# Optimization experiments

Measured on AMD Instinct MI355X. Metric: run time of the kernel, lower is better.

Reference implementation:

```python
import jax, jax.numpy as jnp
import numpy as np

N = 262144          # particles
E = N * 32          # neighbor pairs (edges)


def wendland(q, h):
    # 2D Wendland C2 kernel, q = r/h in [0,1]
    C = 7.0 / (np.pi) / (h * h)
    b = jnp.clip(1.0 - q, 0.0, None)
    return C * (b ** 4) * (1.0 + 4.0 * q)


def setup_inputs() -> dict:
    key = jax.random.key(0)
    k1, k2, k3, k4, k5 = jax.random.split(key, 5)
    area = jax.random.uniform(k1, (N,), jnp.float32) * 0.5 + 0.5
    density = jax.random.uniform(k2, (N,), jnp.float32) * 0.2 + 0.9
    restDensity = jnp.ones((N,), jnp.float32) * 998.0
    velocity = jax.random.normal(k3, (N, 2), jnp.float32)
    radialDistance = jax.random.uniform(k4, (E,), jnp.float32)
    neighbors = jax.random.randint(k5, (2, E), 0, N, jnp.int64)
    return {
        "fluidCoefficient": jnp.float32(0.01),
        "area": area,
        "density": density,
        "restDensity": restDensity,
        "velocity": velocity,
        "radialDistance": radialDistance,
        "neighbors": neighbors,
        "support": jnp.float32(0.02),
    }


def reference(fluidCoefficient, area, density, restDensity, velocity,
              radialDistance, neighbors, support):
    i = neighbors[0]
    j = neighbors[1]
    fac = fluidCoefficient * restDensity[j] * area[j]           # [E]
    rho_i = density[i] * restDensity[i]                          # [E]
    rho_j = density[j] * restDensity[j]                          # [E]
    v_ij = velocity[j] - velocity[i]                             # [E,2]
    k = wendland(radialDistance, support)                        # [E]
    term = (fac / (rho_i + rho_j) * 2.0 * k)[:, None] * v_ij     # [E,2]
    correction = jax.ops.segment_sum(term, i, num_segments=area.shape[0])
    return correction
```

## Files before the change

kernel.cpp:

```cpp
#include <hip/hip_runtime.h>
#include <math.h>

#ifndef M_PI
#define M_PI 3.14159265358979323846
#endif

#define NBLK 512
#define BSZ  512
#define BSH  9

__global__ void detect_idx_width(const unsigned* __restrict__ words,
                                 int* __restrict__ flag) {
    if (blockIdx.x == 0 && threadIdx.x == 0) {
        int is64 = 1;
#pragma unroll 1
        for (int k = 1; k < 2048; k += 2) {
            if (words[k] != 0u) { is64 = 0; break; }
        }
        *flag = is64;
    }
}

__global__ __launch_bounds__(256) void precompute_particle(
    const float* __restrict__ fc_p, const float* __restrict__ area,
    const float* __restrict__ density, const float* __restrict__ restDensity,
    const float* __restrict__ velocity, float4* __restrict__ pre, int N)
{
    int p = blockIdx.x * 256 + threadIdx.x;
    if (p >= N) return;
    const float fc = fc_p[0];
    const float rD = restDensity[p];
    const float2 v = ((const float2*)velocity)[p];
    pre[p] = make_float4(fc * rD * area[p], density[p] * rD, v.x, v.y);
}

__global__ __launch_bounds__(256) void pass_count(
    const void* __restrict__ nbr, const int* __restrict__ flag,
    unsigned* __restrict__ table, int E, int NBnum)
{
    __shared__ unsigned cnt[1024];
    for (int t = threadIdx.x; t < NBnum; t += 256) cnt[t] = 0u;
    __syncthreads();
    const int is64 = *flag;
    const long long chunk = ((long long)E + NBLK - 1) / NBLK;
    const long long s = (long long)blockIdx.x * chunk;
    long long e = s + chunk; if (e > E) e = E;
    if (is64) {
        const long long* ni = (const long long*)nbr;
        for (long long idx = s + threadIdx.x; idx < e; idx += 256) {
            int i = (int)ni[idx];
            atomicAdd(&cnt[i >> BSH], 1u);
        }
    } else {
        const int* ni = (const int*)nbr;
        for (long long idx = s + threadIdx.x; idx < e; idx += 256) {
            int i = ni[idx];
            atomicAdd(&cnt[i >> BSH], 1u);
        }
    }
    __syncthreads();
    for (int t = threadIdx.x; t < NBnum; t += 256)
        table[(size_t)t * NBLK + blockIdx.x] = cnt[t];
}

__global__ __launch_bounds__(NBLK) void scan_blocks(
    unsigned* __restrict__ table, unsigned* __restrict__ btot)
{
    __shared__ unsigned buf[NBLK];
    const int t = threadIdx.x;
    const size_t row = (size_t)blockIdx.x * NBLK;
    buf[t] = table[row + t];
    __syncthreads();
    for (int off = 1; off < NBLK; off <<= 1) {
        unsigned v = (t >= off) ? buf[t - off] : 0u;
        __syncthreads();
        buf[t] += v;
        __syncthreads();
    }
    table[row + t] = (t == 0) ? 0u : buf[t - 1];
    if (t == NBLK - 1) btot[blockIdx.x] = buf[t];
}

__global__ void scan_buckets(const unsigned* __restrict__ btot,
                             unsigned* __restrict__ bstart, int NBnum)
{
    __shared__ unsigned buf[1024];
    const int t = threadIdx.x;
    buf[t] = btot[t];
    __syncthreads();
    for (int off = 1; off < NBnum; off <<= 1) {
        unsigned v = (t >= off) ? buf[t - off] : 0u;
        __syncthreads();
        buf[t] += v;
        __syncthreads();
    }
    bstart[t] = (t == 0) ? 0u : buf[t - 1];
    if (t == NBnum - 1) bstart[NBnum] = buf[t];
}

__global__ __launch_bounds__(256) void pass_scatter(
    const void* __restrict__ nbr, const float* __restrict__ rad,
    const int* __restrict__ flag, const unsigned* __restrict__ table,
    const unsigned* __restrict__ bstart, int2* __restrict__ jq,
    int E, int NBnum)
{
    __shared__ unsigned cur[1024];
    for (int t = threadIdx.x; t < NBnum; t += 256)
        cur[t] = bstart[t] + table[(size_t)t * NBLK + blockIdx.x];
    __syncthreads();
    const int is64 = *flag;
    const long long chunk = ((long long)E + NBLK - 1) / NBLK;
    const long long s = (long long)blockIdx.x * chunk;
    long long e = s + chunk; if (e > E) e = E;
    if (is64) {
        const long long* ni = (const long long*)nbr;
        const long long* nj = ni + E;
        for (long long idx = s + threadIdx.x; idx < e; idx += 256) {
            int i = (int)ni[idx];
            int j = (int)nj[idx];
            float q = rad[idx];
            unsigned pos = atomicAdd(&cur[i >> BSH], 1u);
            jq[pos] = make_int2(j | ((i & (BSZ - 1)) << 22), __float_as_int(q));
        }
    } else {
        const int* ni = (const int*)nbr;
        const int* nj = ni + E;
        for (long long idx = s + threadIdx.x; idx < e; idx += 256) {
            int i = ni[idx];
            int j = nj[idx];
            float q = rad[idx];
            unsigned pos = atomicAdd(&cur[i >> BSH], 1u);
            jq[pos] = make_int2(j | ((i & (BSZ - 1)) << 22), __float_as_int(q));
        }
    }
}

__global__ __launch_bounds__(256) void pass_reduce(
    const int2* __restrict__ jq, const float4* __restrict__ pre,
    const unsigned* __restrict__ bstart, const float* __restrict__ support_p,
    float2* __restrict__ out, int N)
{
    __shared__ float4 plds[BSZ];
    __shared__ float2 acc[BSZ];
    const int k = blockIdx.x;
    const int base = k << BSH;
    for (int t = threadIdx.x; t < BSZ; t += 256) {
        int p = base + t;
        plds[t] = (p < N) ? pre[p] : make_float4(0.f, 0.f, 0.f, 0.f);
        acc[t] = make_float2(0.f, 0.f);
    }
    __syncthreads();
    const float h = support_p[0];
    const float C = 7.0f / ((float)M_PI * h * h);
    const unsigned s = bstart[k];
    const unsigned e = bstart[k + 1];
    for (unsigned idx = s + threadIdx.x; idx < e; idx += 256) {
        const int2 pk = jq[idx];
        const int j = pk.x & ((1 << 22) - 1);
        const int il = (pk.x >> 22) & (BSZ - 1);
        const float q = __int_as_float(pk.y);
        const float4 pj = pre[j];
        const float4 pi = plds[il];
        const float b = fmaxf(1.0f - q, 0.0f);
        const float b2 = b * b;
        const float w = C * (b2 * b2) * fmaf(4.0f, q, 1.0f);
        const float sc = pj.x * 2.0f * w / (pi.y + pj.y);
        atomicAdd(&acc[il].x, sc * (pj.z - pi.z));
        atomicAdd(&acc[il].y, sc * (pj.w - pi.w));
    }
    __syncthreads();
    for (int t = threadIdx.x; t < BSZ; t += 256) {
        int p = base + t;
        if (p < N) out[p] = acc[t];
    }
}

__global__ __launch_bounds__(256) void xsph_edge_kernel(
    const float* __restrict__ fc_p, const float* __restrict__ area,
    const float* __restrict__ density, const float* __restrict__ restDensity,
    const float* __restrict__ velocity, const float* __restrict__ rad,
    const void* __restrict__ nbr, const float* __restrict__ support_p,
    const int* __restrict__ flag, float* __restrict__ out, int E)
{
    const int is64 = *flag;
    const float fc = fc_p[0];
    const float h = support_p[0];
    const float C = 7.0f / ((float)M_PI * h * h);
    const long long e0 =
        (long long)(blockIdx.x * (long long)blockDim.x + threadIdx.x) * 4;
    if (e0 >= (long long)E) return;
    int ii[4], jj[4];
    if (is64) {
        const long long* ni = (const long long*)nbr;
        const long long* nj = ni + E;
#pragma unroll
        for (int k = 0; k < 4; ++k) { ii[k] = (int)ni[e0 + k]; jj[k] = (int)nj[e0 + k]; }
    } else {
        const int* ni = (const int*)nbr;
        const int* nj = ni + E;
        int4 iv = *(const int4*)(ni + e0);
        int4 jv = *(const int4*)(nj + e0);
        ii[0] = iv.x; ii[1] = iv.y; ii[2] = iv.z; ii[3] = iv.w;
        jj[0] = jv.x; jj[1] = jv.y; jj[2] = jv.z; jj[3] = jv.w;
    }
    float4 qv = *(const float4*)(rad + e0);
    float qq[4] = {qv.x, qv.y, qv.z, qv.w};
#pragma unroll
    for (int k = 0; k < 4; ++k) {
        const int i = ii[k], j = jj[k];
        const float rDi = restDensity[i], rDj = restDensity[j];
        const float fac = fc * rDj * area[j];
        const float rho_i = density[i] * rDi, rho_j = density[j] * rDj;
        const float2 vi = *(const float2*)(velocity + 2 * i);
        const float2 vj = *(const float2*)(velocity + 2 * j);
        const float q = qq[k];
        const float b = fmaxf(1.0f - q, 0.0f);
        const float b2 = b * b;
        const float w = C * (b2 * b2) * fmaf(4.0f, q, 1.0f);
        const float s = fac * 2.0f * w / (rho_i + rho_j);
        unsafeAtomicAdd(&out[2 * i],     s * (vj.x - vi.x));
        unsafeAtomicAdd(&out[2 * i + 1], s * (vj.y - vi.y));
    }
}

extern "C" void kernel_launch(void* const* d_in, const int* in_sizes, int n_in,
                              void* d_out, int out_size, void* d_ws, size_t ws_size,
                              hipStream_t stream) {
    const float* fc          = (const float*)d_in[0];
    const float* area        = (const float*)d_in[1];
    const float* density     = (const float*)d_in[2];
    const float* restDensity = (const float*)d_in[3];
    const float* velocity    = (const float*)d_in[4];
    const float* rad         = (const float*)d_in[5];
    const void*  nbr         = d_in[6];
    const float* support     = (const float*)d_in[7];

    const int N = in_sizes[1];
    const int E = in_sizes[5];
    const int NBnum = (N + BSZ - 1) / BSZ;

    char* ws = (char*)d_ws;
    size_t off = 0;
    int* flag = (int*)(ws + off);               off += 16;
    float4* pre = (float4*)(ws + off);          off += (size_t)N * 16;
    unsigned* table = (unsigned*)(ws + off);    off += (size_t)NBnum * NBLK * 4;
    off = (off + 15) & ~(size_t)15;
    unsigned* btot = (unsigned*)(ws + off);     off += (size_t)NBnum * 4;
    off = (off + 15) & ~(size_t)15;
    unsigned* bstart = (unsigned*)(ws + off);   off += (size_t)(NBnum + 1) * 4;
    off = (off + 15) & ~(size_t)15;
    int2* jq = (int2*)(ws + off);               off += (size_t)E * 8;
    const size_t need = off;

    detect_idx_width<<<1, 1, 0, stream>>>((const unsigned*)nbr, flag);

    const bool can_sort =
        (ws_size >= need) && (NBnum <= 1024) && (N <= (1 << 22)) && (E > 0);

    if (can_sort) {
        precompute_particle<<<(N + 255) / 256, 256, 0, stream>>>(
            fc, area, density, restDensity, velocity, pre, N);
        pass_count<<<NBLK, 256, 0, stream>>>(nbr, flag, table, E, NBnum);
        scan_blocks<<<NBnum, NBLK, 0, stream>>>(table, btot);
        scan_buckets<<<1, NBnum, 0, stream>>>(btot, bstart, NBnum);
        pass_scatter<<<NBLK, 256, 0, stream>>>(nbr, rad, flag, table, bstart,
                                               jq, E, NBnum);
        pass_reduce<<<NBnum, 256, 0, stream>>>(jq, pre, bstart, support,
                                               (float2*)d_out, N);
    } else {
        hipMemsetAsync(d_out, 0, (size_t)out_size * sizeof(float), stream);
        const int threads = 256;
        const long long nthreads = ((long long)E + 3) / 4;
        const int blocks = (int)((nthreads + threads - 1) / threads);
        xsph_edge_kernel<<<blocks, threads, 0, stream>>>(
            fc, area, density, restDensity, velocity, rad, nbr, support, flag,
            (float*)d_out, E);
    }
}
```

Before: 219.3 us.

## Stage scatter through LDS local sort for coalesced bucket writes

The scatter pass now counts and locally sorts each block's chunk of edges by bucket in shared memory, then writes them out contiguously per bucket. Before, each edge was written straight to a scattered global slot. The goal is to turn random 8-byte global writes into mostly coalesced runs. Block count rises to 1024 with 8192-edge chunks, and the count table is transposed to be block-major. The cost is re-reading the i indices, 64KB of LDS per block (lower occupancy), and a binary search per output element.

Measured after the change: 229.0 us. 1.04x slower.

```diff
diff --git a/kernel.cpp b/kernel.cpp
--- a/kernel.cpp
+++ b/kernel.cpp
@@ -5,9 +5,11 @@
 #define M_PI 3.14159265358979323846
 #endif
 
-#define NBLK 512
-#define BSZ  512
-#define BSH  9
+#define NBLK  1024
+#define CHUNK 8192
+#define BSZ   512
+#define BSH   9
+#define NBK   512
 
 __global__ void detect_idx_width(const unsigned* __restrict__ words,
                                  int* __restrict__ flag) {
@@ -36,49 +38,44 @@
 
 __global__ __launch_bounds__(256) void pass_count(
     const void* __restrict__ nbr, const int* __restrict__ flag,
-    unsigned* __restrict__ table, int E, int NBnum)
-{
-    __shared__ unsigned cnt[1024];
+    unsigned* __restrict__ table, int E, int chunk, int NBnum)
+{
+    __shared__ unsigned cnt[NBK];
     for (int t = threadIdx.x; t < NBnum; t += 256) cnt[t] = 0u;
     __syncthreads();
     const int is64 = *flag;
-    const long long chunk = ((long long)E + NBLK - 1) / NBLK;
     const long long s = (long long)blockIdx.x * chunk;
     long long e = s + chunk; if (e > E) e = E;
     if (is64) {
         const long long* ni = (const long long*)nbr;
-        for (long long idx = s + threadIdx.x; idx < e; idx += 256) {
-            int i = (int)ni[idx];
-            atomicAdd(&cnt[i >> BSH], 1u);
-        }
+        for (long long idx = s + threadIdx.x; idx < e; idx += 256)
+            atomicAdd(&cnt[((int)ni[idx]) >> BSH], 1u);
     } else {
         const int* ni = (const int*)nbr;
-        for (long long idx = s + threadIdx.x; idx < e; idx += 256) {
-            int i = ni[idx];
-            atomicAdd(&cnt[i >> BSH], 1u);
-        }
+        for (long long idx = s + threadIdx.x; idx < e; idx += 256)
+            atomicAdd(&cnt[ni[idx] >> BSH], 1u);
     }
     __syncthreads();
     for (int t = threadIdx.x; t < NBnum; t += 256)
-        table[(size_t)t * NBLK + blockIdx.x] = cnt[t];
+        table[(size_t)blockIdx.x * NBnum + t] = cnt[t];
 }
 
 __global__ __launch_bounds__(NBLK) void scan_blocks(
-    unsigned* __restrict__ table, unsigned* __restrict__ btot)
+    unsigned* __restrict__ table, unsigned* __restrict__ btot, int NBnum)
 {
     __shared__ unsigned buf[NBLK];
     const int t = threadIdx.x;
-    const size_t row = (size_t)blockIdx.x * NBLK;
-    buf[t] = table[row + t];
-    __syncthreads();
-    for (int off = 1; off < NBLK; off <<= 1) {
-        unsigned v = (t >= off) ? buf[t - off] : 0u;
+    const int k = blockIdx.x;
+    buf[t] = table[(size_t)t * NBnum + k];
+    __syncthreads();
+    for (int o = 1; o < NBLK; o <<= 1) {
+        unsigned v = (t >= o) ? buf[t - o] : 0u;
         __syncthreads();
         buf[t] += v;
         __syncthreads();
     }
-    table[row + t] = (t == 0) ? 0u : buf[t - 1];
-    if (t == NBLK - 1) btot[blockIdx.x] = buf[t];
+    table[(size_t)t * NBnum + k] = (t == 0) ? 0u : buf[t - 1];
+    if (t == NBLK - 1) btot[k] = buf[t];
 }
 
 __global__ void scan_buckets(const unsigned* __restrict__ btot,
@@ -88,8 +85,8 @@
     const int t = threadIdx.x;
     buf[t] = btot[t];
     __syncthreads();
-    for (int off = 1; off < NBnum; off <<= 1) {
-        unsigned v = (t >= off) ? buf[t - off] : 0u;
+    for (int o = 1; o < NBnum; o <<= 1) {
+        unsigned v = (t >= o) ? buf[t - o] : 0u;
         __syncthreads();
         buf[t] += v;
         __syncthreads();
@@ -102,36 +99,87 @@
     const void* __restrict__ nbr, const float* __restrict__ rad,
     const int* __restrict__ flag, const unsigned* __restrict__ table,
     const unsigned* __restrict__ bstart, int2* __restrict__ jq,
-    int E, int NBnum)
-{
-    __shared__ unsigned cur[1024];
-    for (int t = threadIdx.x; t < NBnum; t += 256)
-        cur[t] = bstart[t] + table[(size_t)t * NBLK + blockIdx.x];
-    __syncthreads();
+    int E, int chunk, int NBnum)
+{
+    __shared__ int2 buf[CHUNK];
+    __shared__ unsigned cur[NBK];
+    __shared__ unsigned loff[NBK + 1];
+    __shared__ unsigned dst[NBK];
+
+    const int b = blockIdx.x;
+    const long long s = (long long)b * chunk;
+    long long e = s + chunk; if (e > E) e = E;
+    const int n = (int)(e - s);
+    if (n <= 0) return;
+    const int tid = threadIdx.x;
+
+    for (int k = tid; k < NBnum; k += 256) cur[k] = 0u;
+    __syncthreads();
+
     const int is64 = *flag;
-    const long long chunk = ((long long)E + NBLK - 1) / NBLK;
-    const long long s = (long long)blockIdx.x * chunk;
-    long long e = s + chunk; if (e > E) e = E;
+    if (is64) {
+        const long long* ni = (const long long*)nbr;
+        for (long long idx = s + tid; idx < e; idx += 256)
+            atomicAdd(&cur[((int)ni[idx]) >> BSH], 1u);
+    } else {
+        const int* ni = (const int*)nbr;
+        for (long long idx = s + tid; idx < e; idx += 256)
+            atomicAdd(&cur[ni[idx] >> BSH], 1u);
+    }
+    __syncthreads();
+
+    for (int o = 1; o < NBnum; o <<= 1) {
+        const int t0 = tid, t1 = tid + 256;
+        unsigned v0 = (t0 < NBnum) ? cur[t0] : 0u;
+        unsigned m0 = (t0 >= o && t0 < NBnum) ? cur[t0 - o] : 0u;
+        unsigned v1 = (t1 < NBnum) ? cur[t1] : 0u;
+        unsigned m1 = (t1 >= o && t1 < NBnum) ? cur[t1 - o] : 0u;
+        __syncthreads();
+        if (t0 < NBnum) cur[t0] = v0 + m0;
+        if (t1 < NBnum) cur[t1] = v1 + m1;
+        __syncthreads();
+    }
+    for (int k = tid; k < NBnum; k += 256) {
+        loff[k] = k ? cur[k - 1] : 0u;
+        dst[k] = bstart[k] + table[(size_t)b * NBnum + k];
+    }
+    if (tid == 0) loff[NBnum] = (unsigned)n;
+    __syncthreads();
+    for (int k = tid; k < NBnum; k += 256) cur[k] = loff[k];
+    __syncthreads();
+
     if (is64) {
         const long long* ni = (const long long*)nbr;
         const long long* nj = ni + E;
-        for (long long idx = s + threadIdx.x; idx < e; idx += 256) {
+        for (long long idx = s + tid; idx < e; idx += 256) {
             int i = (int)ni[idx];
             int j = (int)nj[idx];
             float q = rad[idx];
             unsigned pos = atomicAdd(&cur[i >> BSH], 1u);
-            jq[pos] = make_int2(j | ((i & (BSZ - 1)) << 22), __float_as_int(q));
+            buf[pos] = make_int2(j | ((i & (BSZ - 1)) << 22),
+                                 __float_as_int(q));
         }
     } else {
         const int* ni = (const int*)nbr;
         const int* nj = ni + E;
-        for (long long idx = s + threadIdx.x; idx < e; idx += 256) {
+        for (long long idx = s + tid; idx < e; idx += 256) {
             int i = ni[idx];
             int j = nj[idx];
             float q = rad[idx];
             unsigned pos = atomicAdd(&cur[i >> BSH], 1u);
-            jq[pos] = make_int2(j | ((i & (BSZ - 1)) << 22), __float_as_int(q));
+            buf[pos] = make_int2(j | ((i & (BSZ - 1)) << 22),
+                                 __float_as_int(q));
         }
+    }
+    __syncthreads();
+
+    for (int t = tid; t < n; t += 256) {
+        int lo = 0, hi = NBnum;
+        while (hi - lo > 1) {
+            int mid = (lo + hi) >> 1;
+            if (loff[mid] <= (unsigned)t) lo = mid; else hi = mid;
+        }
+        jq[dst[lo] + ((unsigned)t - loff[lo])] = buf[t];
     }
 }
 
@@ -238,12 +286,13 @@
     const int N = in_sizes[1];
     const int E = in_sizes[5];
     const int NBnum = (N + BSZ - 1) / BSZ;
+    const int chunk = (int)(((long long)E + NBLK - 1) / NBLK);
 
     char* ws = (char*)d_ws;
     size_t off = 0;
     int* flag = (int*)(ws + off);               off += 16;
     float4* pre = (float4*)(ws + off);          off += (size_t)N * 16;
-    unsigned* table = (unsigned*)(ws + off);    off += (size_t)NBnum * NBLK * 4;
+    unsigned* table = (unsigned*)(ws + off);    off += (size_t)NBLK * NBnum * 4;
     off = (off + 15) & ~(size_t)15;
     unsigned* btot = (unsigned*)(ws + off);     off += (size_t)NBnum * 4;
     off = (off + 15) & ~(size_t)15;
@@ -255,16 +304,17 @@
     detect_idx_width<<<1, 1, 0, stream>>>((const unsigned*)nbr, flag);
 
     const bool can_sort =
-        (ws_size >= need) && (NBnum <= 1024) && (N <= (1 << 22)) && (E > 0);
+        (ws_size >= need) && (NBnum <= NBK) && (N <= (1 << 22)) &&
+        (chunk <= CHUNK) && (E > 0);
 
     if (can_sort) {
         precompute_particle<<<(N + 255) / 256, 256, 0, stream>>>(
             fc, area, density, restDensity, velocity, pre, N);
-        pass_count<<<NBLK, 256, 0, stream>>>(nbr, flag, table, E, NBnum);
-        scan_blocks<<<NBnum, NBLK, 0, stream>>>(table, btot);
+        pass_count<<<NBLK, 256, 0, stream>>>(nbr, flag, table, E, chunk, NBnum);
+        scan_blocks<<<NBnum, NBLK, 0, stream>>>(table, btot, NBnum);
         scan_buckets<<<1, NBnum, 0, stream>>>(btot, bstart, NBnum);
         pass_scatter<<<NBLK, 256, 0, stream>>>(nbr, rad, flag, table, bstart,
-                                               jq, E, NBnum);
+                                               jq, E, chunk, NBnum);
         pass_reduce<<<NBnum, 256, 0, stream>>>(jq, pre, bstart, support,
                                                (float2*)d_out, N);
     } else {
```
